# Kernel optimization log

Hardware: AMD Instinct MI355X
Metric: run time of the kernel (lower is better)

Reference implementation:

```python
import jax, jax.numpy as jnp
import numpy as np

B, S, D_IN, D, H = 2, 2048, 1024, 1024, 16
HD = D // H

def setup_inputs() -> dict:
    key = jax.random.key(0)
    k1, k2, k3 = jax.random.split(key, 3)
    # xavier_uniform-style scale for weights
    lim_qkv = float(np.sqrt(6.0 / (D_IN + 3 * D)))
    lim_o = float(np.sqrt(6.0 / (D + D)))
    return {
        "x": jax.random.normal(k1, (B, S, D_IN), dtype=jnp.float32),
        "w_qkv": jax.random.uniform(k2, (3 * D, D_IN), dtype=jnp.float32, minval=-lim_qkv, maxval=lim_qkv),
        "b_qkv": jnp.zeros((3 * D,), dtype=jnp.float32),
        "w_o": jax.random.uniform(k3, (D, D), dtype=jnp.float32, minval=-lim_o, maxval=lim_o),
        "b_o": jnp.zeros((D,), dtype=jnp.float32),
    }

def reference(x, w_qkv, b_qkv, w_o, b_o):
    b, s, _ = x.shape
    # QKV projection: [B,S,3D]
    qkv = jnp.einsum("bsd,ed->bse", x, w_qkv) + b_qkv
    # [B,S,H,3*HD] -> [B,H,S,3*HD]
    qkv = qkv.reshape(b, s, H, 3 * HD).transpose(0, 2, 1, 3)
    q, k, v = jnp.split(qkv, 3, axis=-1)  # each [B,H,S,HD]
    scale = 1.0 / jnp.sqrt(jnp.asarray(HD, dtype=q.dtype))
    logits = jnp.einsum("bhqd,bhkd->bhqk", q, k) * scale  # [B,H,S,S]
    attn = jax.nn.softmax(logits, axis=-1)
    vals = jnp.einsum("bhqk,bhkd->bhqd", attn, v)  # [B,H,S,HD]
    vals = vals.transpose(0, 2, 1, 3).reshape(b, s, D)
    return jnp.einsum("bsd,ed->bse", vals, w_o) + b_o
```

## Files before the change

kernel.cpp:

```cpp
#include <hip/hip_runtime.h>
#include <hip/hip_bf16.h>
#include <math.h>

#define BATCH 2
#define SLEN  2048
#define DIN   1024
#define DMODEL 1024
#define NHEAD 16
#define HD    64
#define E3    3072

typedef unsigned short us;
typedef _Float16 f16;
typedef __attribute__((ext_vector_type(8))) _Float16 f16x8;
typedef __attribute__((ext_vector_type(8))) unsigned short us8;
typedef __attribute__((ext_vector_type(4))) unsigned short us4;
typedef __attribute__((ext_vector_type(4))) float f32x4;
typedef __attribute__((ext_vector_type(16))) float f32x16;
typedef __attribute__((ext_vector_type(4))) unsigned int u32x4;

#define QSCALE 0.18033688011112042f

__device__ __forceinline__ us f16bits(float x) {
    const f16 h = (f16)x;
    return __builtin_bit_cast(us, h);
}

__device__ __forceinline__ unsigned int pkrtz(float a, float b) {
    return __builtin_bit_cast(unsigned int, __builtin_amdgcn_cvt_pkrtz(a, b));
}

__device__ __forceinline__ void plswap(unsigned int& a, unsigned int& b) {
    asm volatile("v_permlane32_swap_b32 %0, %1" : "+v"(a), "+v"(b));
}

__device__ __forceinline__ void barrier_raw() {
    asm volatile("s_barrier" ::: "memory");
}

#define GLL16(g, l)                                                                     \
    __builtin_amdgcn_global_load_lds((const __attribute__((address_space(1))) unsigned int*)(g), \
                                     (__attribute__((address_space(3))) unsigned int*)(l), 16, 0, 0)

__global__ __launch_bounds__(256) void cvt3_f16(
    const float* __restrict__ x, us* __restrict__ ox, int nx,
    const float* __restrict__ wq, us* __restrict__ owq, int nq,
    const float* __restrict__ wo, us* __restrict__ owo)
{
    int i = (blockIdx.x * 256 + threadIdx.x) * 8;
    const float* s;
    us* o;
    if (i < nx)           { s = x;  o = ox; }
    else if (i < nx + nq) { s = wq; o = owq; i -= nx; }
    else                  { s = wo; o = owo; i -= nx + nq; }
    const float4 f0 = *(const float4*)&s[i];
    const float4 f1 = *(const float4*)&s[i + 4];
    const float v[8] = {f0.x, f0.y, f0.z, f0.w, f1.x, f1.y, f1.z, f1.w};
    us8 h;
#pragma unroll
    for (int j = 0; j < 8; ++j) h[j] = f16bits(v[j]);
    *(us8*)&o[i] = h;
}

#define GBK 64
#define GNT (DIN / GBK)

template <int BN, bool QKV_OUT>
__global__ __launch_bounds__(256) void gemm_db(
    const us* __restrict__ Am, const us* __restrict__ Bm,
    const float* __restrict__ bias, void* __restrict__ Cout,
    int M, int N, int K)
{
    constexpr int NJ  = BN / 32;
    constexpr int BGL = BN / 32;
    __shared__ __align__(16) us ldsA[2 * 128 * 64];
    __shared__ __align__(16) us ldsB[2 * BN * 64];

    const int t    = threadIdx.x;
    const int lane = t & 63;
    const int w    = t >> 6;
    const int ml   = lane & 15;
    const int quad = lane >> 4;
    const int msk  = ml & 7;
    const int wm   = w >> 1;
    const int wn   = w & 1;

    const int nbx = N / BN;
    const int nwg = (M >> 7) * nbx;
    int wg = blockIdx.y * nbx + blockIdx.x;
    wg = (wg & 7) * (nwg >> 3) + (wg >> 3);
    const int m0 = (wg / nbx) * 128;
    const int n0 = (wg % nbx) * BN;

    const int r8  = lane >> 3;
    const int xsw = ((lane & 7) ^ r8) * 8;
    const us* pA = Am + (size_t)(m0 + w * 32 + r8) * K + xsw;
    const int brow = (BN == 128) ? w * 32 : w * 16;
    const us* pB = Bm + (size_t)(n0 + brow + r8) * K + xsw;

#define STG_A(d, kk) do { _Pragma("unroll") for (int g = 0; g < 4; ++g) \
    GLL16(pA + (size_t)(8 * g) * K + (kk), &ldsA[(d) * 8192 + w * 2048 + g * 512]); } while (0)
#define STG_B(d, kk) do { _Pragma("unroll") for (int g = 0; g < BGL; ++g) \
    GLL16(pB + (size_t)(8 * g) * K + (kk), &ldsB[(d) * (BN * 64) + brow * 64 + g * 512]); } while (0)

#define LDA(d, mi, ks) __builtin_bit_cast(f16x8, *(const us8*)&ldsA[(d) * 8192 + (wm * 64 + (mi) * 16 + ml) * 64 + (((quad ^ msk) ^ ((ks) << 2)) * 8)])
#define LDB(d, nj, ks) __builtin_bit_cast(f16x8, *(const us8*)&ldsB[(d) * (BN * 64) + (wn * (BN / 2) + (nj) * 16 + ml) * 64 + (((quad ^ msk) ^ ((ks) << 2)) * 8)])

#define WAIT_BGL() do { if constexpr (BN == 128) asm volatile("s_waitcnt vmcnt(4)" ::: "memory"); \
                        else                     asm volatile("s_waitcnt vmcnt(2)" ::: "memory"); } while (0)

    f32x4 acc[4][NJ];
#pragma unroll
    for (int i = 0; i < 4; ++i)
#pragma unroll
        for (int j = 0; j < NJ; ++j) {
            acc[i][j][0] = 0.f; acc[i][j][1] = 0.f; acc[i][j][2] = 0.f; acc[i][j][3] = 0.f;
        }

    STG_A(0, 0); STG_B(0, 0);
    STG_B(1, GBK);
    WAIT_BGL();
    barrier_raw();

    for (int tt = 0; tt < GNT; ++tt) {
        const int d = tt & 1, e = d ^ 1;

        if (tt + 1 < GNT) STG_A(e, (tt + 1) * GBK);
        f16x8 bf[2][NJ];
#pragma unroll
        for (int ks = 0; ks < 2; ++ks)
#pragma unroll
            for (int nj = 0; nj < NJ; ++nj)
                bf[ks][nj] = LDB(d, nj, ks);
        f16x8 a0[2][2];
#pragma unroll
        for (int mi = 0; mi < 2; ++mi) {
            a0[mi][0] = LDA(d, mi, 0);
            a0[mi][1] = LDA(d, mi, 1);
        }
        __builtin_amdgcn_s_setprio(1);
#pragma unroll
        for (int ks = 0; ks < 2; ++ks)
#pragma unroll
            for (int nj = 0; nj < NJ; ++nj)
#pragma unroll
                for (int mi = 0; mi < 2; ++mi)
                    acc[mi][nj] = __builtin_amdgcn_mfma_f32_16x16x32_f16(a0[mi][ks], bf[ks][nj], acc[mi][nj], 0, 0, 0);
        __builtin_amdgcn_s_setprio(0);
        barrier_raw();

        if (tt + 2 < GNT) STG_B(d, (tt + 2) * GBK);
        f16x8 a1[2][2];
#pragma unroll
        for (int mi = 0; mi < 2; ++mi) {
            a1[mi][0] = LDA(d, mi + 2, 0);
            a1[mi][1] = LDA(d, mi + 2, 1);
        }
        __builtin_amdgcn_s_setprio(1);
#pragma unroll
        for (int ks = 0; ks < 2; ++ks)
#pragma unroll
            for (int nj = 0; nj < NJ; ++nj)
#pragma unroll
                for (int mi = 0; mi < 2; ++mi)
                    acc[mi + 2][nj] = __builtin_amdgcn_mfma_f32_16x16x32_f16(a1[mi][ks], bf[ks][nj], acc[mi + 2][nj], 0, 0, 0);
        __builtin_amdgcn_s_setprio(0);

        if (tt + 2 < GNT)      WAIT_BGL();
        else if (tt + 1 < GNT) asm volatile("s_waitcnt vmcnt(0)" ::: "memory");
        barrier_raw();
    }

    float bj[NJ], cs[NJ];
#pragma unroll
    for (int nj = 0; nj < NJ; ++nj) {
        const int col = n0 + wn * (BN / 2) + nj * 16 + ml;
        bj[nj] = bias[col];
        cs[nj] = (QKV_OUT && (col % 192) < 64) ? QSCALE : 1.0f;
    }
#pragma unroll
    for (int mi = 0; mi < 4; ++mi) {
#pragma unroll
        for (int r = 0; r < 4; ++r) {
            const size_t rowoff = (size_t)(m0 + wm * 64 + mi * 16 + quad * 4 + r) * N;
#pragma unroll
            for (int nj = 0; nj < NJ; ++nj) {
                const int col = n0 + wn * (BN / 2) + nj * 16 + ml;
                const float v = (acc[mi][nj][r] + bj[nj]) * cs[nj];
                if (QKV_OUT) ((us*)Cout)[rowoff + col] = f16bits(v);
                else         ((float*)Cout)[rowoff + col] = v;
            }
        }
    }
#undef STG_A
#undef STG_B
#undef LDA
#undef LDB
#undef WAIT_BGL
}

#define ABQ 128
#define ACH 64
#define NCH (SLEN / ACH)
#define NCH2 (NCH / 2)
#define LQA 72
#define OSTR 68

__global__ __launch_bounds__(512, 4) void attn_mfma(
    const us* __restrict__ qkvh, us* __restrict__ vals)
{
    __shared__ __align__(16) us smem[36864];
    us* const Qs = smem;
    us* const Ks = smem + 9216;
    us* const Vt = smem + 18432;

    const int t    = threadIdx.x;
    const int lane = t & 63;
    const int w    = t >> 6;
    const int sp   = w >> 2;
    const int wq4  = w & 3;
    const int t2   = t & 255;
    const int m32  = lane & 31;
    const int half = lane >> 5;

    const int wg  = blockIdx.x;
    const int s9  = wg >> 3;
    const int bh  = ((s9 >> 4) << 3) | (wg & 7);
    const int b   = bh >> 4;
    const int h   = bh & 15;
    const int q0  = (s9 & 15) * ABQ;

    const size_t base = (size_t)b * SLEN * E3;
    const int qoff = h * 192;

    const int krA = t2 >> 2;
    const int ksA = (t2 & 3) * 16;
    const int k2  = t2 & 31;
    const int d0v = (t2 >> 5) * 8;

    us* const myK  = Ks + sp * 4608;
    us* const myV0 = Vt + sp * 4608;
    us* const myV1 = Vt + 9216 + sp * 4608;
    const int cg0 = sp * NCH2;

    {
        const int row = t >> 2;
        const int c0q = (t & 3) * 16;
        const us* g = &qkvh[base + (size_t)(q0 + row) * E3 + qoff + c0q];
        *(us8*)&Qs[row * LQA + c0q]     = *(const us8*)g;
        *(us8*)&Qs[row * LQA + c0q + 8] = *(const us8*)(g + 8);
    }

    us8 kk0, kk1, vv0, vv1;
    {
        const us* gK = &qkvh[base + (size_t)(cg0 * ACH + krA) * E3 + qoff + 64 + ksA];
        kk0 = *(const us8*)gK; kk1 = *(const us8*)(gK + 8);
        const us* gV = &qkvh[base + (size_t)(cg0 * ACH + 2 * k2) * E3 + qoff + 128 + d0v];
        vv0 = *(const us8*)gV; vv1 = *(const us8*)(gV + E3);
    }
    *(us8*)&myK[krA * LQA + ksA]     = kk0;
    *(us8*)&myK[krA * LQA + ksA + 8] = kk1;
#pragma unroll
    for (int j = 0; j < 8; ++j) {
        const unsigned int pv = (unsigned int)vv0[j] | ((unsigned int)vv1[j] << 16);
        *(unsigned int*)&myV0[(d0v + j) * LQA + 2 * k2] = pv;
    }
    if (1 < NCH2) {
        const int cg = cg0 + 1;
        const us* gK = &qkvh[base + (size_t)(cg * ACH + krA) * E3 + qoff + 64 + ksA];
        kk0 = *(const us8*)gK; kk1 = *(const us8*)(gK + 8);
        const us* gV = &qkvh[base + (size_t)(cg * ACH + 2 * k2) * E3 + qoff + 128 + d0v];
        vv0 = *(const us8*)gV; vv1 = *(const us8*)(gV + E3);
    }
    __syncthreads();

    f16x8 aq[4];
#pragma unroll
    for (int s = 0; s < 4; ++s)
        aq[s] = __builtin_bit_cast(f16x8, *(const us8*)&Qs[(wq4 * 32 + m32) * LQA + half * 8 + 16 * s]);

    f32x16 O[2];
#pragma unroll
    for (int dt = 0; dt < 2; ++dt)
#pragma unroll
        for (int r = 0; r < 16; ++r) O[dt][r] = 0.f;
    float lp[4] = {0.f, 0.f, 0.f, 0.f};

    for (int c = 0; c < NCH2; ++c) {
        us* const Vrd = (c & 1) ? myV1 : myV0;
        us* const Vwr = (c & 1) ? myV0 : myV1;

        if (c + 1 < NCH2) {
#pragma unroll
            for (int j = 0; j < 8; ++j) {
                const unsigned int pv = (unsigned int)vv0[j] | ((unsigned int)vv1[j] << 16);
                *(unsigned int*)&Vwr[(d0v + j) * LQA + 2 * k2] = pv;
            }
        }

        f16x8 pf[4];
#pragma unroll
        for (int kt = 0; kt < 2; ++kt) {
            f32x16 z;
#pragma unroll
            for (int r = 0; r < 16; ++r) z[r] = 0.f;
#pragma unroll
            for (int s = 0; s < 4; ++s) {
                const f16x8 ak = __builtin_bit_cast(f16x8, *(const us8*)&myK[(kt * 32 + m32) * LQA + half * 8 + 16 * s]);
                z = __builtin_amdgcn_mfma_f32_32x32x16_f16(ak, aq[s], z, 0, 0, 0);
            }
            float p[16];
#pragma unroll
            for (int r = 0; r < 16; ++r) {
                p[r] = __builtin_amdgcn_exp2f(z[r]);
                lp[r & 3] += p[r];
            }
            unsigned int a0 = pkrtz(p[0],  p[1]),  a1 = pkrtz(p[2],  p[3]);
            unsigned int b0 = pkrtz(p[4],  p[5]),  b1 = pkrtz(p[6],  p[7]);
            plswap(a0, b0); plswap(a1, b1);
            pf[2 * kt] = __builtin_bit_cast(f16x8, (u32x4){a0, a1, b0, b1});
            unsigned int e0 = pkrtz(p[8],  p[9]),  e1 = pkrtz(p[10], p[11]);
            unsigned int f0 = pkrtz(p[12], p[13]), f1 = pkrtz(p[14], p[15]);
            plswap(e0, f0); plswap(e1, f1);
            pf[2 * kt + 1] = __builtin_bit_cast(f16x8, (u32x4){e0, e1, f0, f1});
        }

        __syncthreads();

        if (c + 1 < NCH2) {
            *(us8*)&myK[krA * LQA + ksA]     = kk0;
            *(us8*)&myK[krA * LQA + ksA + 8] = kk1;
        }
        if (c + 2 < NCH2) {
            const int cg = cg0 + c + 2;
            const us* gK = &qkvh[base + (size_t)(cg * ACH + krA) * E3 + qoff + 64 + ksA];
            kk0 = *(const us8*)gK; kk1 = *(const us8*)(gK + 8);
            const us* gV = &qkvh[base + (size_t)(cg * ACH + 2 * k2) * E3 + qoff + 128 + d0v];
            vv0 = *(const us8*)gV; vv1 = *(const us8*)(gV + E3);
        }

#pragma unroll
        for (int dt = 0; dt < 2; ++dt) {
#pragma unroll
            for (int s = 0; s < 4; ++s) {
                const f16x8 av = __builtin_bit_cast(f16x8, *(const us8*)&Vrd[(dt * 32 + m32) * LQA + half * 8 + 16 * s]);
                O[dt] = __builtin_amdgcn_mfma_f32_32x32x16_f16(av, pf[s], O[dt], 0, 0, 0);
            }
        }

        __syncthreads();
    }

    const float lpart = (lp[0] + lp[1]) + (lp[2] + lp[3]);
    const float l = lpart + __shfl_xor(lpart, 32);
    const int ql = wq4 * 32 + m32;

    __syncthreads();
    float* const Osc = (float*)smem;
    float* const lsc = Osc + ABQ * OSTR;

    if (sp == 1) {
#pragma unroll
        for (int dt = 0; dt < 2; ++dt) {
#pragma unroll
            for (int g = 0; g < 4; ++g) {
                const f32x4 o4 = {O[dt][g * 4], O[dt][g * 4 + 1], O[dt][g * 4 + 2], O[dt][g * 4 + 3]};
                *(f32x4*)&Osc[ql * OSTR + dt * 32 + 8 * g + 4 * half] = o4;
            }
        }
        if (half == 0) lsc[ql] = l;
    }
    __syncthreads();
    if (sp == 0) {
        const float rl = 1.0f / (l + lsc[ql]);
        const int sq = q0 + ql;
        const size_t rowbase = (size_t)(b * SLEN + sq) * DMODEL + h * HD;
#pragma unroll
        for (int dt = 0; dt < 2; ++dt) {
#pragma unroll
            for (int g = 0; g < 4; ++g) {
                const f32x4 part = *(const f32x4*)&Osc[ql * OSTR + dt * 32 + 8 * g + 4 * half];
                us4 o4;
#pragma unroll
                for (int r2 = 0; r2 < 4; ++r2)
                    o4[r2] = f16bits((O[dt][g * 4 + r2] + part[r2]) * rl);
                *(us4*)&vals[rowbase + dt * 32 + 8 * g + 4 * half] = o4;
            }
        }
    }
}

extern "C" void kernel_launch(void* const* d_in, const int* in_sizes, int n_in,
                              void* d_out, int out_size, void* d_ws, size_t ws_size,
                              hipStream_t stream) {
    const float* x     = (const float*)d_in[0];
    const float* w_qkv = (const float*)d_in[1];
    const float* b_qkv = (const float*)d_in[2];
    const float* w_o   = (const float*)d_in[3];
    const float* b_o   = (const float*)d_in[4];
    float* out = (float*)d_out;

    const int M   = BATCH * SLEN;
    const int XN  = M * DIN;
    const int WQN = E3 * DIN;
    const int WON = DMODEL * DMODEL;
    const size_t QKVN = (size_t)BATCH * SLEN * E3;

    us* qkvh = (us*)d_ws;
    us* xh   = qkvh + QKVN;
    us* wq   = xh + XN;
    us* wo   = wq + WQN;

    cvt3_f16<<<dim3((XN + WQN + WON) / 2048), 256, 0, stream>>>(
        x, xh, XN, w_qkv, wq, WQN, w_o, wo);

    gemm_db<128, true><<<dim3(E3 / 128, M / 128), 256, 0, stream>>>(
        xh, wq, b_qkv, qkvh, M, E3, DIN);

    us* vals = xh;
    attn_mfma<<<dim3((SLEN / ABQ) * BATCH * NHEAD), 512, 0, stream>>>(qkvh, vals);

    gemm_db<64, false><<<dim3(DMODEL / 64, M / 128), 256, 0, stream>>>(
        vals, wo, b_o, out, M, DMODEL, DMODEL);
}
```

Baseline: 186.6 us.

## Load K fragments straight from global into registers, drop K LDS staging and a barrier

Each wave now reads its K MFMA operand fragments directly from global memory into registers, replacing the staging of K through shared memory. This shrinks LDS use and removes one __syncthreads per chunk, since only the V double buffer needs a barrier. The trade-off is that every wave redundantly loads the full K chunk from global/L2, with less coalesced row-strided reads, and holds more registers for K, which may pressure occupancy at 512 threads.

Result: slower. 231.5 us (+24.1%).

```diff
diff --git a/kernel.cpp b/kernel.cpp
--- a/kernel.cpp
+++ b/kernel.cpp
@@ -209,10 +209,10 @@
 __global__ __launch_bounds__(512, 4) void attn_mfma(
     const us* __restrict__ qkvh, us* __restrict__ vals)
 {
-    __shared__ __align__(16) us smem[36864];
+    __shared__ __align__(16) us smem[27648];
     us* const Qs = smem;
-    us* const Ks = smem + 9216;
-    us* const Vt = smem + 18432;
+    us* const Vb0 = smem + 9216;
+    us* const Vb1 = smem + 18432;
 
     const int t    = threadIdx.x;
     const int lane = t & 63;
@@ -233,15 +233,19 @@
     const size_t base = (size_t)b * SLEN * E3;
     const int qoff = h * 192;
 
-    const int krA = t2 >> 2;
-    const int ksA = (t2 & 3) * 16;
     const int k2  = t2 & 31;
     const int d0v = (t2 >> 5) * 8;
 
-    us* const myK  = Ks + sp * 4608;
-    us* const myV0 = Vt + sp * 4608;
-    us* const myV1 = Vt + 9216 + sp * 4608;
+    us* const myV0 = Vb0 + sp * 4608;
+    us* const myV1 = Vb1 + sp * 4608;
     const int cg0 = sp * NCH2;
+
+    const us* const gK = &qkvh[base + (size_t)m32 * E3 + qoff + 64 + half * 8];
+
+    us8 kr[2][4];
+#define LOADK(cgi) do { _Pragma("unroll") for (int kt = 0; kt < 2; ++kt) \
+    _Pragma("unroll") for (int s = 0; s < 4; ++s) \
+        kr[kt][s] = *(const us8*)&gK[(size_t)((cgi) * ACH + kt * 32) * E3 + 16 * s]; } while (0)
 
     {
         const int row = t >> 2;
@@ -251,25 +255,19 @@
         *(us8*)&Qs[row * LQA + c0q + 8] = *(const us8*)(g + 8);
     }
 
-    us8 kk0, kk1, vv0, vv1;
+    LOADK(cg0);
+    us8 vv0, vv1;
     {
-        const us* gK = &qkvh[base + (size_t)(cg0 * ACH + krA) * E3 + qoff + 64 + ksA];
-        kk0 = *(const us8*)gK; kk1 = *(const us8*)(gK + 8);
         const us* gV = &qkvh[base + (size_t)(cg0 * ACH + 2 * k2) * E3 + qoff + 128 + d0v];
         vv0 = *(const us8*)gV; vv1 = *(const us8*)(gV + E3);
     }
-    *(us8*)&myK[krA * LQA + ksA]     = kk0;
-    *(us8*)&myK[krA * LQA + ksA + 8] = kk1;
 #pragma unroll
     for (int j = 0; j < 8; ++j) {
         const unsigned int pv = (unsigned int)vv0[j] | ((unsigned int)vv1[j] << 16);
         *(unsigned int*)&myV0[(d0v + j) * LQA + 2 * k2] = pv;
     }
-    if (1 < NCH2) {
-        const int cg = cg0 + 1;
-        const us* gK = &qkvh[base + (size_t)(cg * ACH + krA) * E3 + qoff + 64 + ksA];
-        kk0 = *(const us8*)gK; kk1 = *(const us8*)(gK + 8);
-        const us* gV = &qkvh[base + (size_t)(cg * ACH + 2 * k2) * E3 + qoff + 128 + d0v];
+    {
+        const us* gV = &qkvh[base + (size_t)((cg0 + 1) * ACH + 2 * k2) * E3 + qoff + 128 + d0v];
         vv0 = *(const us8*)gV; vv1 = *(const us8*)(gV + E3);
     }
     __syncthreads();
@@ -290,14 +288,6 @@
         us* const Vrd = (c & 1) ? myV1 : myV0;
         us* const Vwr = (c & 1) ? myV0 : myV1;
 
-        if (c + 1 < NCH2) {
-#pragma unroll
-            for (int j = 0; j < 8; ++j) {
-                const unsigned int pv = (unsigned int)vv0[j] | ((unsigned int)vv1[j] << 16);
-                *(unsigned int*)&Vwr[(d0v + j) * LQA + 2 * k2] = pv;
-            }
-        }
-
         f16x8 pf[4];
 #pragma unroll
         for (int kt = 0; kt < 2; ++kt) {
@@ -305,10 +295,9 @@
 #pragma unroll
             for (int r = 0; r < 16; ++r) z[r] = 0.f;
 #pragma unroll
-            for (int s = 0; s < 4; ++s) {
-                const f16x8 ak = __builtin_bit_cast(f16x8, *(const us8*)&myK[(kt * 32 + m32) * LQA + half * 8 + 16 * s]);
-                z = __builtin_amdgcn_mfma_f32_32x32x16_f16(ak, aq[s], z, 0, 0, 0);
-            }
+            for (int s = 0; s < 4; ++s)
+                z = __builtin_amdgcn_mfma_f32_32x32x16_f16(
+                        __builtin_bit_cast(f16x8, kr[kt][s]), aq[s], z, 0, 0, 0);
             float p[16];
 #pragma unroll
             for (int r = 0; r < 16; ++r) {
@@ -325,17 +314,17 @@
             pf[2 * kt + 1] = __builtin_bit_cast(f16x8, (u32x4){e0, e1, f0, f1});
         }
 
-        __syncthreads();
+        if (c + 1 < NCH2) LOADK(cg0 + c + 1);
 
         if (c + 1 < NCH2) {
-            *(us8*)&myK[krA * LQA + ksA]     = kk0;
-            *(us8*)&myK[krA * LQA + ksA + 8] = kk1;
+#pragma unroll
+            for (int j = 0; j < 8; ++j) {
+                const unsigned int pv = (unsigned int)vv0[j] | ((unsigned int)vv1[j] << 16);
+                *(unsigned int*)&Vwr[(d0v + j) * LQA + 2 * k2] = pv;
+            }
         }
         if (c + 2 < NCH2) {
-            const int cg = cg0 + c + 2;
-            const us* gK = &qkvh[base + (size_t)(cg * ACH + krA) * E3 + qoff + 64 + ksA];
-            kk0 = *(const us8*)gK; kk1 = *(const us8*)(gK + 8);
-            const us* gV = &qkvh[base + (size_t)(cg * ACH + 2 * k2) * E3 + qoff + 128 + d0v];
+            const us* gV = &qkvh[base + (size_t)((cg0 + c + 2) * ACH + 2 * k2) * E3 + qoff + 128 + d0v];
             vv0 = *(const us8*)gV; vv1 = *(const us8*)(gV + E3);
         }
 
@@ -388,6 +377,7 @@
             }
         }
     }
+#undef LOADK
 }
 
 extern "C" void kernel_launch(void* const* d_in, const int* in_sizes, int n_in,
```
